# Optimization experiments

Hardware: AMD Instinct MI355X
Metric: run time of the kernel (lower is better)

Reference implementation:

```python
import jax, jax.numpy as jnp
import numpy as np

B, T, I, H, O = 256, 100, 1024, 2048, 10

def setup_inputs() -> dict:
    key = jax.random.key(0)
    k = jax.random.split(key, 6)
    return {
        "x": jax.random.normal(k[0], (B, T, I), dtype=jnp.float32),
        "h0": jax.random.normal(k[1], (B, H), dtype=jnp.float32),
        "Win": jax.random.uniform(k[2], (I, H), dtype=jnp.float32, minval=-0.1, maxval=0.1),
        "W": jax.random.normal(k[3], (H, H), dtype=jnp.float32) * 0.01,
        "lin_w": jax.random.normal(k[4], (O, H), dtype=jnp.float32) * 0.02,
        "lin_b": jax.random.normal(k[5], (O,), dtype=jnp.float32) * 0.02,
    }

def reference(x, h0, Win, W, lin_w, lin_b):
    xin = jnp.einsum('bti,ih->bth', x, Win)  # precompute input projection for all steps

    def step(h, xin_t):
        h = jnp.tanh(xin_t + h @ W)
        y = h @ lin_w.T + lin_b
        return h, y

    _, ys = jax.lax.scan(step, h0, jnp.swapaxes(xin, 0, 1))  # ys: [T, B, O]
    return jnp.swapaxes(ys, 0, 1)  # [B, T, O]
```

## Files before the change

### kernel.cpp

```cpp
#include <hip/hip_runtime.h>
#include <math.h>

#define Bn 256
#define Tn 100
#define In 1024
#define Hn 2048
#define On 10
#define Kc (In + Hn)

typedef short s8v  __attribute__((ext_vector_type(8)));
typedef unsigned short us4 __attribute__((ext_vector_type(4)));
typedef float f32x4 __attribute__((ext_vector_type(4)));

__device__ __forceinline__ unsigned short f2bf(float f) {
    unsigned int u = __float_as_uint(f);
    u += 0x7fffu + ((u >> 16) & 1u);
    return (unsigned short)(u >> 16);
}

__device__ __forceinline__ float fast_tanh(float x) {
    float e = __expf(x + x);
    return 1.0f - 2.0f * __builtin_amdgcn_rcpf(e + 1.0f);
}


__global__ void conv_x_kernel(const float4* __restrict__ src, ushort4* __restrict__ dst) {
    int i = blockIdx.x * 256 + threadIdx.x;
    float4 v = src[i];
    ushort4 o;
    o.x = f2bf(v.x); o.y = f2bf(v.y); o.z = f2bf(v.z); o.w = f2bf(v.w);
    dst[i] = o;
}

__global__ void transpose_bf16_kernel(const float* __restrict__ src, unsigned short* __restrict__ dst,
                                      int N, int ld, int colOff) {
    __shared__ float tile[32][33];
    int k0 = blockIdx.x * 32;
    int n0 = blockIdx.y * 32;
    int c = threadIdx.x & 31;
    int r = threadIdx.x >> 5;
    #pragma unroll
    for (int i = 0; i < 32; i += 8)
        tile[r + i][c] = src[(size_t)(k0 + r + i) * N + n0 + c];
    __syncthreads();
    #pragma unroll
    for (int i = 0; i < 32; i += 8)
        dst[(size_t)(n0 + r + i) * ld + colOff + k0 + c] = f2bf(tile[c][r + i]);
}

__global__ void small_conv_kernel(const float* __restrict__ h0, const float* __restrict__ lin_w,
                                  unsigned short* __restrict__ h_all0, unsigned short* __restrict__ lwb,
                                  unsigned int* __restrict__ bar) {
    int idx = blockIdx.x * 256 + threadIdx.x;
    if (idx < 512) bar[idx] = 0u;
    if (idx < Bn * Hn) {
        h_all0[idx] = f2bf(h0[idx]);
    } else {
        int j = idx - Bn * Hn;
        int o = j >> 11;
        int k = j & 2047;
        lwb[j] = (o < On) ? f2bf(lin_w[o * Hn + k]) : (unsigned short)0;
    }
}

__global__ __launch_bounds__(512, 2)
void scan_kernel(const unsigned short* __restrict__ xb,
                 const unsigned short* __restrict__ BTm,
                 unsigned short* __restrict__ h_all,
                 unsigned int* __restrict__ bar) {
    const int g = blockIdx.x;
    const int mg = (g >> 3) & 3;
    const int m0 = mg * 64;
    const int n0 = ((g & 7) * 8 + (g >> 5)) * 32;
    const int w = threadIdx.x >> 6;
    const int lane = threadIdx.x & 63;
    const int quad = lane >> 4;
    const int lr = lane & 15;

    __shared__ float red[4][64][36];

    const unsigned short* bp0 = BTm + (size_t)(n0 + lr) * Kc;
    const unsigned short* bp1 = BTm + (size_t)(n0 + 16 + lr) * Kc;

    const size_t xrow = (size_t)Tn * In;

    unsigned int* grp_cnt = bar + mg * 32;
    unsigned int* gep     = bar + 128 + mg * 32;

    s8v bx[4][2];
    s8v bh[8][2];
    #pragma unroll
    for (int c = 0; c < 4; ++c) {
        const int kq = w * 128 + c * 32 + quad * 8;
        bx[c][0] = *(const s8v*)(bp0 + kq);
        bx[c][1] = *(const s8v*)(bp1 + kq);
    }
    #pragma unroll
    for (int c = 0; c < 8; ++c) {
        const int kq = In + w * 256 + c * 32 + quad * 8;
        bh[c][0] = *(const s8v*)(bp0 + kq);
        bh[c][1] = *(const s8v*)(bp1 + kq);
    }

    f32x4 acc[4][2];
    #pragma unroll
    for (int mi = 0; mi < 4; ++mi)
        #pragma unroll
        for (int ni = 0; ni < 2; ++ni)
            acc[mi][ni] = (f32x4){0.f, 0.f, 0.f, 0.f};

    {
        const unsigned short* xt = xb + 0 * In;
        #pragma unroll
        for (int c = 0; c < 4; ++c) {
            const int kq = w * 128 + c * 32 + quad * 8;
            const unsigned short* arow = xt + kq + (size_t)(m0 + lr) * xrow;
            s8v a0 = *(const s8v*)(arow);
            s8v a1 = *(const s8v*)(arow + 16 * xrow);
            s8v a2 = *(const s8v*)(arow + 32 * xrow);
            s8v a3 = *(const s8v*)(arow + 48 * xrow);
            acc[0][0] = __builtin_amdgcn_mfma_f32_16x16x32_bf16(a0, bx[c][0], acc[0][0], 0, 0, 0);
            acc[1][0] = __builtin_amdgcn_mfma_f32_16x16x32_bf16(a1, bx[c][0], acc[1][0], 0, 0, 0);
            acc[2][0] = __builtin_amdgcn_mfma_f32_16x16x32_bf16(a2, bx[c][0], acc[2][0], 0, 0, 0);
            acc[3][0] = __builtin_amdgcn_mfma_f32_16x16x32_bf16(a3, bx[c][0], acc[3][0], 0, 0, 0);
            acc[0][1] = __builtin_amdgcn_mfma_f32_16x16x32_bf16(a0, bx[c][1], acc[0][1], 0, 0, 0);
            acc[1][1] = __builtin_amdgcn_mfma_f32_16x16x32_bf16(a1, bx[c][1], acc[1][1], 0, 0, 0);
            acc[2][1] = __builtin_amdgcn_mfma_f32_16x16x32_bf16(a2, bx[c][1], acc[2][1], 0, 0, 0);
            acc[3][1] = __builtin_amdgcn_mfma_f32_16x16x32_bf16(a3, bx[c][1], acc[3][1], 0, 0, 0);
        }
    }

    for (int t = 0; t < Tn; ++t) {
        const unsigned short* hrow = h_all + (size_t)t * (Bn * Hn)
                                   + (size_t)(m0 + lr) * Hn + w * 256 + quad * 8;
        s8v A[2][4];
        #pragma unroll
        for (int r = 0; r < 4; ++r)
            A[0][r] = *(const s8v*)(hrow + r * 16 * Hn);
        #pragma unroll
        for (int c = 0; c < 8; ++c) {
            if (c < 7) {
                const unsigned short* p = hrow + (c + 1) * 32;
                #pragma unroll
                for (int r = 0; r < 4; ++r)
                    A[(c + 1) & 1][r] = *(const s8v*)(p + r * 16 * Hn);
            }
            const s8v a0 = A[c & 1][0];
            const s8v a1 = A[c & 1][1];
            const s8v a2 = A[c & 1][2];
            const s8v a3 = A[c & 1][3];
            acc[0][0] = __builtin_amdgcn_mfma_f32_16x16x32_bf16(a0, bh[c][0], acc[0][0], 0, 0, 0);
            acc[1][0] = __builtin_amdgcn_mfma_f32_16x16x32_bf16(a1, bh[c][0], acc[1][0], 0, 0, 0);
            acc[2][0] = __builtin_amdgcn_mfma_f32_16x16x32_bf16(a2, bh[c][0], acc[2][0], 0, 0, 0);
            acc[3][0] = __builtin_amdgcn_mfma_f32_16x16x32_bf16(a3, bh[c][0], acc[3][0], 0, 0, 0);
            acc[0][1] = __builtin_amdgcn_mfma_f32_16x16x32_bf16(a0, bh[c][1], acc[0][1], 0, 0, 0);
            acc[1][1] = __builtin_amdgcn_mfma_f32_16x16x32_bf16(a1, bh[c][1], acc[1][1], 0, 0, 0);
            acc[2][1] = __builtin_amdgcn_mfma_f32_16x16x32_bf16(a2, bh[c][1], acc[2][1], 0, 0, 0);
            acc[3][1] = __builtin_amdgcn_mfma_f32_16x16x32_bf16(a3, bh[c][1], acc[3][1], 0, 0, 0);
        }

        if (w < 4) {
            #pragma unroll
            for (int mi = 0; mi < 4; ++mi)
                #pragma unroll
                for (int ni = 0; ni < 2; ++ni)
                    #pragma unroll
                    for (int rr = 0; rr < 4; ++rr)
                        red[w][mi * 16 + quad * 4 + rr][ni * 16 + lr] = acc[mi][ni][rr];
        }
        __syncthreads();
        if (w >= 4) {
            #pragma unroll
            for (int mi = 0; mi < 4; ++mi)
                #pragma unroll
                for (int ni = 0; ni < 2; ++ni)
                    #pragma unroll
                    for (int rr = 0; rr < 4; ++rr)
                        red[w - 4][mi * 16 + quad * 4 + rr][ni * 16 + lr] += acc[mi][ni][rr];
        }
        __syncthreads();

        {
            int j = threadIdx.x << 2;
            int row = j >> 5;
            int c0 = j & 31;
            float4 s0 = *(const float4*)&red[0][row][c0];
            float4 s1 = *(const float4*)&red[1][row][c0];
            float4 s2 = *(const float4*)&red[2][row][c0];
            float4 s3 = *(const float4*)&red[3][row][c0];
            us4 o4;
            o4[0] = f2bf(fast_tanh(s0.x + s1.x + s2.x + s3.x));
            o4[1] = f2bf(fast_tanh(s0.y + s1.y + s2.y + s3.y));
            o4[2] = f2bf(fast_tanh(s0.z + s1.z + s2.z + s3.z));
            o4[3] = f2bf(fast_tanh(s0.w + s1.w + s2.w + s3.w));
            unsigned long long* dst = (unsigned long long*)
                (h_all + (size_t)(t + 1) * (Bn * Hn) + (size_t)(m0 + row) * Hn + n0 + c0);
            __hip_atomic_store(dst, __builtin_bit_cast(unsigned long long, o4),
                               __ATOMIC_RELAXED, __HIP_MEMORY_SCOPE_AGENT);
        }

        if (t < Tn - 1) {
            __syncthreads();
            const unsigned int tp1 = (unsigned int)(t + 1);

            if (threadIdx.x == 0) {
                unsigned int old = __hip_atomic_fetch_add(grp_cnt, 1u, __ATOMIC_RELAXED,
                                                          __HIP_MEMORY_SCOPE_AGENT);
                if (old == 64u * tp1 - 1u)
                    __hip_atomic_store(gep, tp1, __ATOMIC_RELAXED,
                                       __HIP_MEMORY_SCOPE_AGENT);
            }

            #pragma unroll
            for (int mi = 0; mi < 4; ++mi)
                #pragma unroll
                for (int ni = 0; ni < 2; ++ni)
                    acc[mi][ni] = (f32x4){0.f, 0.f, 0.f, 0.f};
            const unsigned short* xt = xb + (size_t)(t + 1) * In;
            #pragma unroll
            for (int c = 0; c < 4; ++c) {
                const int kq = w * 128 + c * 32 + quad * 8;
                const unsigned short* arow = xt + kq + (size_t)(m0 + lr) * xrow;
                s8v a0 = *(const s8v*)(arow);
                s8v a1 = *(const s8v*)(arow + 16 * xrow);
                s8v a2 = *(const s8v*)(arow + 32 * xrow);
                s8v a3 = *(const s8v*)(arow + 48 * xrow);
                acc[0][0] = __builtin_amdgcn_mfma_f32_16x16x32_bf16(a0, bx[c][0], acc[0][0], 0, 0, 0);
                acc[1][0] = __builtin_amdgcn_mfma_f32_16x16x32_bf16(a1, bx[c][0], acc[1][0], 0, 0, 0);
                acc[2][0] = __builtin_amdgcn_mfma_f32_16x16x32_bf16(a2, bx[c][0], acc[2][0], 0, 0, 0);
                acc[3][0] = __builtin_amdgcn_mfma_f32_16x16x32_bf16(a3, bx[c][0], acc[3][0], 0, 0, 0);
                acc[0][1] = __builtin_amdgcn_mfma_f32_16x16x32_bf16(a0, bx[c][1], acc[0][1], 0, 0, 0);
                acc[1][1] = __builtin_amdgcn_mfma_f32_16x16x32_bf16(a1, bx[c][1], acc[1][1], 0, 0, 0);
                acc[2][1] = __builtin_amdgcn_mfma_f32_16x16x32_bf16(a2, bx[c][1], acc[2][1], 0, 0, 0);
                acc[3][1] = __builtin_amdgcn_mfma_f32_16x16x32_bf16(a3, bx[c][1], acc[3][1], 0, 0, 0);
            }

            if (lane == 0) {
                while (__hip_atomic_load(gep, __ATOMIC_RELAXED,
                                         __HIP_MEMORY_SCOPE_AGENT) < tp1)
                    __builtin_amdgcn_s_sleep(2);
            }
            asm volatile("" ::: "memory");
        }
    }
}

__global__ __launch_bounds__(256)
void gemm2_kernel(const unsigned short* __restrict__ h_all, const unsigned short* __restrict__ lwb,
                  const float* __restrict__ lb, float* __restrict__ y) {
    int gw = blockIdx.x * 4 + (threadIdx.x >> 6);
    int lane = threadIdx.x & 63, quad = lane >> 4, lr = lane & 15;
    int m0 = gw * 16;
    int t = m0 >> 8;
    int b0 = m0 & 255;
    const unsigned short* ah = h_all + ((size_t)(t + 1) * Bn + b0 + lr) * Hn + quad * 8;
    const unsigned short* bh = lwb + (size_t)lr * Hn + quad * 8;
    f32x4 acc0 = {0.f, 0.f, 0.f, 0.f}, acc1 = {0.f, 0.f, 0.f, 0.f};
    #pragma unroll
    for (int k0 = 0; k0 < Hn; k0 += 64) {
        s8v a0 = *(const s8v*)(ah + k0);
        s8v b0 = *(const s8v*)(bh + k0);
        acc0 = __builtin_amdgcn_mfma_f32_16x16x32_bf16(a0, b0, acc0, 0, 0, 0);
        s8v a1 = *(const s8v*)(ah + k0 + 32);
        s8v b1 = *(const s8v*)(bh + k0 + 32);
        acc1 = __builtin_amdgcn_mfma_f32_16x16x32_bf16(a1, b1, acc1, 0, 0, 0);
    }
    acc0 = acc0 + acc1;
    if (lr < On) {
        float bias = lb[lr];
        #pragma unroll
        for (int rr = 0; rr < 4; ++rr) {
            int b = b0 + quad * 4 + rr;
            y[(size_t)b * (Tn * On) + t * On + lr] = acc0[rr] + bias;
        }
    }
}


extern "C" void kernel_launch(void* const* d_in, const int* in_sizes, int n_in,
                              void* d_out, int out_size, void* d_ws, size_t ws_size,
                              hipStream_t stream) {
    const float* x   = (const float*)d_in[0];
    const float* h0  = (const float*)d_in[1];
    const float* Win = (const float*)d_in[2];
    const float* W   = (const float*)d_in[3];
    const float* lw  = (const float*)d_in[4];
    const float* lb  = (const float*)d_in[5];
    float* y = (float*)d_out;

    unsigned short* ws    = (unsigned short*)d_ws;
    unsigned short* xb    = ws;
    unsigned short* BTm   = xb + (size_t)Bn * Tn * In;
    unsigned short* h_all = BTm + (size_t)Hn * Kc;
    unsigned short* lwb   = h_all + (size_t)(Tn + 1) * Bn * Hn;
    unsigned int*   bar   = (unsigned int*)(lwb + 32768);

    conv_x_kernel<<<25600, 256, 0, stream>>>((const float4*)x, (ushort4*)xb);
    transpose_bf16_kernel<<<dim3(32, 64), 256, 0, stream>>>(Win, BTm, Hn, Kc, 0);
    transpose_bf16_kernel<<<dim3(64, 64), 256, 0, stream>>>(W, BTm, Hn, Kc, In);
    small_conv_kernel<<<2176, 256, 0, stream>>>(h0, lw, h_all, lwb, bar);

    scan_kernel<<<256, 512, 0, stream>>>(xb, BTm, h_all, bar);

    gemm2_kernel<<<400, 256, 0, stream>>>(h_all, lwb, lb, y);
}
```

Baseline: 1.426 ms.

## Replace counter barrier with per-block flags and single-pass LDS reduction

```diff
diff --git a/kernel.cpp b/kernel.cpp
--- a/kernel.cpp
+++ b/kernel.cpp
@@ -77,15 +77,15 @@
     const int quad = lane >> 4;
     const int lr = lane & 15;
 
-    __shared__ float red[4][64][36];
+    __shared__ float red[8][64][36];
 
     const unsigned short* bp0 = BTm + (size_t)(n0 + lr) * Kc;
     const unsigned short* bp1 = BTm + (size_t)(n0 + 16 + lr) * Kc;
 
     const size_t xrow = (size_t)Tn * In;
 
-    unsigned int* grp_cnt = bar + mg * 32;
-    unsigned int* gep     = bar + 128 + mg * 32;
+    const int fidx = mg * 64 + (g & 7) * 8 + (g >> 5);
+    unsigned int* fl = bar + mg * 64;
 
     s8v bx[4][2];
     s8v bh[8][2];
@@ -159,25 +159,13 @@
             acc[3][1] = __builtin_amdgcn_mfma_f32_16x16x32_bf16(a3, bh[c][1], acc[3][1], 0, 0, 0);
         }
 
-        if (w < 4) {
+        #pragma unroll
+        for (int mi = 0; mi < 4; ++mi)
             #pragma unroll
-            for (int mi = 0; mi < 4; ++mi)
+            for (int ni = 0; ni < 2; ++ni)
                 #pragma unroll
-                for (int ni = 0; ni < 2; ++ni)
-                    #pragma unroll
-                    for (int rr = 0; rr < 4; ++rr)
-                        red[w][mi * 16 + quad * 4 + rr][ni * 16 + lr] = acc[mi][ni][rr];
-        }
-        __syncthreads();
-        if (w >= 4) {
-            #pragma unroll
-            for (int mi = 0; mi < 4; ++mi)
-                #pragma unroll
-                for (int ni = 0; ni < 2; ++ni)
-                    #pragma unroll
-                    for (int rr = 0; rr < 4; ++rr)
-                        red[w - 4][mi * 16 + quad * 4 + rr][ni * 16 + lr] += acc[mi][ni][rr];
-        }
+                for (int rr = 0; rr < 4; ++rr)
+                    red[w][mi * 16 + quad * 4 + rr][ni * 16 + lr] = acc[mi][ni][rr];
         __syncthreads();
 
         {
@@ -188,11 +176,15 @@
             float4 s1 = *(const float4*)&red[1][row][c0];
             float4 s2 = *(const float4*)&red[2][row][c0];
             float4 s3 = *(const float4*)&red[3][row][c0];
+            float4 s4 = *(const float4*)&red[4][row][c0];
+            float4 s5 = *(const float4*)&red[5][row][c0];
+            float4 s6 = *(const float4*)&red[6][row][c0];
+            float4 s7 = *(const float4*)&red[7][row][c0];
             us4 o4;
-            o4[0] = f2bf(fast_tanh(s0.x + s1.x + s2.x + s3.x));
-            o4[1] = f2bf(fast_tanh(s0.y + s1.y + s2.y + s3.y));
-            o4[2] = f2bf(fast_tanh(s0.z + s1.z + s2.z + s3.z));
-            o4[3] = f2bf(fast_tanh(s0.w + s1.w + s2.w + s3.w));
+            o4[0] = f2bf(fast_tanh(((s0.x + s1.x) + (s2.x + s3.x)) + ((s4.x + s5.x) + (s6.x + s7.x))));
+            o4[1] = f2bf(fast_tanh(((s0.y + s1.y) + (s2.y + s3.y)) + ((s4.y + s5.y) + (s6.y + s7.y))));
+            o4[2] = f2bf(fast_tanh(((s0.z + s1.z) + (s2.z + s3.z)) + ((s4.z + s5.z) + (s6.z + s7.z))));
+            o4[3] = f2bf(fast_tanh(((s0.w + s1.w) + (s2.w + s3.w)) + ((s4.w + s5.w) + (s6.w + s7.w))));
             unsigned long long* dst = (unsigned long long*)
                 (h_all + (size_t)(t + 1) * (Bn * Hn) + (size_t)(m0 + row) * Hn + n0 + c0);
             __hip_atomic_store(dst, __builtin_bit_cast(unsigned long long, o4),
@@ -203,13 +195,9 @@
             __syncthreads();
             const unsigned int tp1 = (unsigned int)(t + 1);
 
-            if (threadIdx.x == 0) {
-                unsigned int old = __hip_atomic_fetch_add(grp_cnt, 1u, __ATOMIC_RELAXED,
-                                                          __HIP_MEMORY_SCOPE_AGENT);
-                if (old == 64u * tp1 - 1u)
-                    __hip_atomic_store(gep, tp1, __ATOMIC_RELAXED,
-                                       __HIP_MEMORY_SCOPE_AGENT);
-            }
+            if (threadIdx.x == 0)
+                __hip_atomic_store(bar + fidx, tp1, __ATOMIC_RELAXED,
+                                   __HIP_MEMORY_SCOPE_AGENT);
 
             #pragma unroll
             for (int mi = 0; mi < 4; ++mi)
@@ -235,10 +223,11 @@
                 acc[3][1] = __builtin_amdgcn_mfma_f32_16x16x32_bf16(a3, bx[c][1], acc[3][1], 0, 0, 0);
             }
 
-            if (lane == 0) {
-                while (__hip_atomic_load(gep, __ATOMIC_RELAXED,
-                                         __HIP_MEMORY_SCOPE_AGENT) < tp1)
-                    __builtin_amdgcn_s_sleep(2);
+            while (true) {
+                unsigned int v = __hip_atomic_load(fl + lane, __ATOMIC_RELAXED,
+                                                   __HIP_MEMORY_SCOPE_AGENT);
+                if (__all((int)(v >= tp1))) break;
+                __builtin_amdgcn_s_sleep(1);
             }
             asm volatile("" ::: "memory");
         }
```

After: 1.375 ms. -3.6%, faster.
